# Kernel tuning notes

Measured on AMD Instinct MI355X. Metric: run time of the kernel, lower is better.

## Reference

```python
import jax, jax.numpy as jnp
import numpy as np

N = 1_000_000          # number of fusion candidate pairs
H, W = 200, 70400      # sparse buffer dims hard-coded in the module
FILL = -9999999.0


def _init_conv(k, co, ci):
    # torch Conv2d default init: U(-1/sqrt(fan_in), 1/sqrt(fan_in)), 1x1 kernel
    bound = 1.0 / np.sqrt(ci)
    kw, kb = jax.random.split(k)
    w = jax.random.uniform(kw, (co, ci), jnp.float32, -bound, bound)
    b = jax.random.uniform(kb, (co,), jnp.float32, -bound, bound)
    return w, b


def setup_inputs() -> dict:
    key = jax.random.key(0)
    ks = jax.random.split(key, 7)
    input_1 = jax.random.normal(ks[0], (1, 4, 1, N), dtype=jnp.float32)
    idx0 = jax.random.randint(ks[1], (N,), 0, H)   # row in [0,200)
    idx1 = jax.random.randint(ks[2], (N,), 0, W)   # col in [0,70400)
    tensor_index = jnp.stack([idx0, idx1], axis=1).astype(jnp.int64)
    w1, b1 = _init_conv(ks[3], 18, 4)
    w2, b2 = _init_conv(ks[4], 36, 18)
    w3, b3 = _init_conv(ks[5], 36, 36)
    w4, b4 = _init_conv(ks[6], 1, 36)
    return dict(input_1=input_1, tensor_index=tensor_index,
                w1=w1, b1=b1, w2=w2, b2=b2, w3=w3, b3=b3, w4=w4, b4=b4)


def _fuse_2d_3d(x, w1, b1, w2, b2, w3, b3, w4, b4):
    # x: (4, N); 1x1 convs over a (1,C,1,N) tensor == per-point channel matmuls
    h = jax.nn.relu(w1 @ x + b1[:, None])
    h = jax.nn.relu(w2 @ h + b2[:, None])
    h = jax.nn.relu(w3 @ h + b3[:, None])
    return w4 @ h + b4[:, None]  # (1, N)


def reference(input_1, tensor_index, w1, b1, w2, b2, w3, b3, w4, b4):
    base = jnp.full((1, H, W), FILL, dtype=input_1.dtype)

    def scatter_branch(_):
        feat = _fuse_2d_3d(input_1[0, :, 0, :], w1, b1, w2, b2, w3, b3, w4, b4)  # (1, N)
        out = base.at[:, tensor_index[:, 0], tensor_index[:, 1]].set(feat)
        return out, jnp.int32(1)

    def empty_branch(_):
        return base, jnp.int32(0)

    out_1, flag = jax.lax.cond(tensor_index[0, 0] == -1,
                               empty_branch, scatter_branch, None)
    # MaxPool2d([200,1]) over (C=1,H=200,W) -> max over H; squeeze+reshape -> (1, W, 1)
    x = jnp.max(out_1, axis=1)            # (1, W)
    return x.reshape(1, -1, 1), flag
```

## Files before the change

### kernel.cpp

```cpp
#include <hip/hip_runtime.h>

#define N_PTS 1000000
#define H_DIM 200
#define W_DIM 70400
#define FILL_V -9999999.0f

typedef float v2f __attribute__((ext_vector_type(2)));

__device__ __forceinline__ v2f fma2(v2f a, v2f b, v2f c) {
    return __builtin_elementwise_fma(a, b, c);
}

__global__ void __launch_bounds__(512) mlp_scatter_kernel(
    const float* __restrict__ input,
    const int* __restrict__ tindex,
    const float* __restrict__ w1, const float* __restrict__ b1,
    const float* __restrict__ w2, const float* __restrict__ b2,
    const float* __restrict__ w3, const float* __restrict__ b3,
    const float* __restrict__ w4, const float* __restrict__ b4,
    int* __restrict__ counts,
    uint2* __restrict__ list,
    int maxk)
{
    if (tindex[0] == -1) return;

    const int i = blockIdx.x * 512 + threadIdx.x;
    if (i >= N_PTS) return;

    const int2 hw = ((const int2*)tindex)[i];
    const int pos = atomicAdd(&counts[hw.y], 1);

    const v2f* __restrict__ w1v = (const v2f*)w1;
    const v2f* __restrict__ w2v = (const v2f*)w2;
    const v2f* __restrict__ w3v = (const v2f*)w3;

    const v2f x01 = { input[0 * N_PTS + i], input[1 * N_PTS + i] };
    const v2f x23 = { input[2 * N_PTS + i], input[3 * N_PTS + i] };

    v2f h1v[9];
#pragma unroll
    for (int o = 0; o < 18; ++o) {
        v2f acc = { b1[o], 0.0f };
        acc = fma2(w1v[o * 2 + 0], x01, acc);
        acc = fma2(w1v[o * 2 + 1], x23, acc);
        const float h = fmaxf(acc.x + acc.y, 0.0f);
        if (o & 1) h1v[o >> 1].y = h; else h1v[o >> 1].x = h;
    }

    v2f h2v[18];
#pragma unroll
    for (int o = 0; o < 36; ++o) {
        v2f acc = { b2[o], 0.0f };
#pragma unroll
        for (int q = 0; q < 9; ++q)
            acc = fma2(w2v[o * 9 + q], h1v[q], acc);
        const float h = fmaxf(acc.x + acc.y, 0.0f);
        if (o & 1) h2v[o >> 1].y = h; else h2v[o >> 1].x = h;
    }

    float v = b4[0];
#pragma unroll
    for (int o = 0; o < 36; ++o) {
        v2f acc = { b3[o], 0.0f };
#pragma unroll
        for (int q = 0; q < 18; ++q)
            acc = fma2(w3v[o * 18 + q], h2v[q], acc);
        v = fmaf(w4[o], fmaxf(acc.x + acc.y, 0.0f), v);
    }

    if (pos < maxk) {
        uint2 e;
        e.x = __float_as_uint(v);
        e.y = ((unsigned)i << 8) | (unsigned)hw.x;
        list[(size_t)hw.y * maxk + pos] = e;
    }
}

__device__ __forceinline__ void lds_wave_fence() {
    asm volatile("s_waitcnt lgkmcnt(0)" ::: "memory");
}

__global__ void __launch_bounds__(256) colmax_kernel(
    const int* __restrict__ tindex,
    const int* __restrict__ counts,
    const uint2* __restrict__ list,
    float* __restrict__ out,
    int maxk)
{
    __shared__ unsigned rowwin[4][200];
    const int lane = threadIdx.x;
    const int y    = threadIdx.y;
    unsigned* tbl = rowwin[y];

    const bool empty = (tindex[0] == -1);

    if (blockIdx.x == 0 && lane == 0 && y == 0)
        out[W_DIM] = empty ? 0.0f : 1.0f;

    tbl[lane]       = 0u;
    tbl[lane + 64]  = 0u;
    tbl[lane + 128] = 0u;
    if (lane < 8) tbl[lane + 192] = 0u;
    lds_wave_fence();

    const int step = gridDim.x * 4;
    for (int w = blockIdx.x * 4 + y; w < W_DIM; w += step) {
        int c = 0;
        if (!empty) {
            c = counts[w];
            if (c > maxk) c = maxk;
        }

        uint2 e = make_uint2(0u, 0u);
        const bool have = (lane < c);
        float v = FILL_V;
        if (have) {
            e = list[(size_t)w * maxk + lane];
            atomicMax(&tbl[e.y & 0xFFu], e.y);
        }
        lds_wave_fence();
        if (have) {
            if (tbl[e.y & 0xFFu] == e.y)
                v = __uint_as_float(e.x);
            tbl[e.y & 0xFFu] = 0u;
        }
        lds_wave_fence();

#pragma unroll
        for (int off = 32; off > 0; off >>= 1)
            v = fmaxf(v, __shfl_down(v, off, 64));

        if (lane == 0) out[w] = v;
    }
}

extern "C" void kernel_launch(void* const* d_in, const int* in_sizes, int n_in,
                              void* d_out, int out_size, void* d_ws, size_t ws_size,
                              hipStream_t stream) {
    const float* input  = (const float*)d_in[0];
    const int*   tindex = (const int*)d_in[1];
    const float* w1 = (const float*)d_in[2];
    const float* b1 = (const float*)d_in[3];
    const float* w2 = (const float*)d_in[4];
    const float* b2 = (const float*)d_in[5];
    const float* w3 = (const float*)d_in[6];
    const float* b3 = (const float*)d_in[7];
    const float* w4 = (const float*)d_in[8];
    const float* b4 = (const float*)d_in[9];
    float* out = (float*)d_out;

    int*   counts = (int*)d_ws;
    uint2* list   = (uint2*)((char*)d_ws + (size_t)W_DIM * sizeof(int));

    size_t avail = (ws_size > (size_t)W_DIM * sizeof(int))
                       ? ws_size - (size_t)W_DIM * sizeof(int) : 0;
    int maxk = (int)(avail / ((size_t)W_DIM * sizeof(uint2)));
    if (maxk > 64) maxk = 64;
    if (maxk < 1)  maxk = 1;

    (void)hipMemsetAsync(counts, 0, (size_t)W_DIM * sizeof(int), stream);

    mlp_scatter_kernel<<<(N_PTS + 511) / 512, 512, 0, stream>>>(
        input, tindex, w1, b1, w2, b2, w3, b3, w4, b4, counts, list, maxk);

    colmax_kernel<<<2200, dim3(64, 4), 0, stream>>>(
        tindex, counts, list, out, maxk);
}
```

Measured before the change: 174.5 us.

## Run per-point MLP on bf16 MFMA with packed weights and bias folding

Replaces the per-thread FP32 FMA evaluation of the 4→18→36→36→1 MLP with bf16 MFMA 16x16x32 instructions. Each wavefront processes 64 points, and activations are shuffled between layers with ds_bpermute. A small pre-kernel packs the weights into MFMA fragment layout, with the biases folded in as an extra input column set to 1. The aim is to cut the VALU cost of the MLP, at the price of bf16 rounding of weights and activations, an extra kernel launch, and heavy cross-lane permute traffic.

```diff
diff --git a/kernel.cpp b/kernel.cpp
--- a/kernel.cpp
+++ b/kernel.cpp
@@ -5,72 +5,200 @@
 #define W_DIM 70400
 #define FILL_V -9999999.0f
 
-typedef float v2f __attribute__((ext_vector_type(2)));
-
-__device__ __forceinline__ v2f fma2(v2f a, v2f b, v2f c) {
-    return __builtin_elementwise_fma(a, b, c);
-}
-
-__global__ void __launch_bounds__(512) mlp_scatter_kernel(
-    const float* __restrict__ input,
-    const int* __restrict__ tindex,
+#define COUNTS_BYTES ((size_t)W_DIM * sizeof(int))
+#define WPACK_ELEMS  6656
+#define WPACK_BYTES  ((size_t)WPACK_ELEMS * 2)
+
+typedef __attribute__((ext_vector_type(4))) float f32x4;
+typedef __attribute__((ext_vector_type(8))) short bf16x8;
+
+__device__ __forceinline__ unsigned bperm_u(unsigned src_lane, unsigned v) {
+    return (unsigned)__builtin_amdgcn_ds_bpermute((int)(src_lane << 2), (int)v);
+}
+__device__ __forceinline__ unsigned cvt_pk_bf16(float lo, float hi) {
+    unsigned d;
+    asm("v_cvt_pk_bf16_f32 %0, %1, %2" : "=v"(d) : "v"(lo), "v"(hi));
+    return d;
+}
+__device__ __forceinline__ bf16x8 mk_frag(unsigned d0, unsigned d1,
+                                          unsigned d2, unsigned d3) {
+    union { unsigned u[4]; bf16x8 s; } u;
+    u.u[0] = d0; u.u[1] = d1; u.u[2] = d2; u.u[3] = d3;
+    return u.s;
+}
+
+__global__ void __launch_bounds__(256) pack_weights_kernel(
     const float* __restrict__ w1, const float* __restrict__ b1,
     const float* __restrict__ w2, const float* __restrict__ b2,
     const float* __restrict__ w3, const float* __restrict__ b3,
     const float* __restrict__ w4, const float* __restrict__ b4,
+    unsigned short* __restrict__ wp)
+{
+    for (int idx = threadIdx.x; idx < WPACK_ELEMS; idx += 256) {
+        const int rem  = idx & 511;
+        const int lane = rem >> 3, j = rem & 7;
+        const int c16 = lane & 15, g = lane >> 4;
+        const int kloc = g * 8 + j;
+        float v = 0.0f;
+        if (idx < 1024) {
+            const int row = (idx >> 9) * 16 + c16, k = kloc;
+            if (row < 18) v = (k < 4) ? w1[row * 4 + k] : (k == 4 ? b1[row] : 0.0f);
+        } else if (idx < 2560) {
+            const int row = ((idx - 1024) >> 9) * 16 + c16, k = kloc;
+            if (row < 36) v = (k < 18) ? w2[row * 18 + k] : (k == 18 ? b2[row] : 0.0f);
+        } else if (idx < 5632) {
+            const int f = (idx - 2560) >> 9;
+            const int row = (f >> 1) * 16 + c16, k = (f & 1) * 32 + kloc;
+            if (row < 36) v = (k < 36) ? w3[row * 36 + k] : (k == 36 ? b3[row] : 0.0f);
+        } else {
+            const int row = c16, k = ((idx - 5632) >> 9) * 32 + kloc;
+            if (row == 0) v = (k < 36) ? w4[k] : (k == 36 ? b4[0] : 0.0f);
+        }
+        const unsigned b = __float_as_uint(v);
+        wp[idx] = (unsigned short)((b + 0x7FFFu + ((b >> 16) & 1u)) >> 16);
+    }
+}
+
+__global__ void __launch_bounds__(256) mlp_scatter_kernel(
+    const float* __restrict__ input,
+    const int* __restrict__ tindex,
+    const unsigned short* __restrict__ wp,
     int* __restrict__ counts,
     uint2* __restrict__ list,
     int maxk)
 {
     if (tindex[0] == -1) return;
 
-    const int i = blockIdx.x * 512 + threadIdx.x;
-    if (i >= N_PTS) return;
+    const int l   = threadIdx.x & 63;
+    const int wav = (blockIdx.x * 256 + threadIdx.x) >> 6;
+    const int base = wav << 6;
+    if (base >= N_PTS) return;
+    const int i = base + l;
+    const int c16 = l & 15, g = l >> 4;
 
     const int2 hw = ((const int2*)tindex)[i];
     const int pos = atomicAdd(&counts[hw.y], 1);
 
-    const v2f* __restrict__ w1v = (const v2f*)w1;
-    const v2f* __restrict__ w2v = (const v2f*)w2;
-    const v2f* __restrict__ w3v = (const v2f*)w3;
-
-    const v2f x01 = { input[0 * N_PTS + i], input[1 * N_PTS + i] };
-    const v2f x23 = { input[2 * N_PTS + i], input[3 * N_PTS + i] };
-
-    v2f h1v[9];
-#pragma unroll
-    for (int o = 0; o < 18; ++o) {
-        v2f acc = { b1[o], 0.0f };
-        acc = fma2(w1v[o * 2 + 0], x01, acc);
-        acc = fma2(w1v[o * 2 + 1], x23, acc);
-        const float h = fmaxf(acc.x + acc.y, 0.0f);
-        if (o & 1) h1v[o >> 1].y = h; else h1v[o >> 1].x = h;
-    }
-
-    v2f h2v[18];
-#pragma unroll
-    for (int o = 0; o < 36; ++o) {
-        v2f acc = { b2[o], 0.0f };
-#pragma unroll
-        for (int q = 0; q < 9; ++q)
-            acc = fma2(w2v[o * 9 + q], h1v[q], acc);
-        const float h = fmaxf(acc.x + acc.y, 0.0f);
-        if (o & 1) h2v[o >> 1].y = h; else h2v[o >> 1].x = h;
-    }
-
-    float v = b4[0];
-#pragma unroll
-    for (int o = 0; o < 36; ++o) {
-        v2f acc = { b3[o], 0.0f };
-#pragma unroll
-        for (int q = 0; q < 18; ++q)
-            acc = fma2(w3v[o * 18 + q], h2v[q], acc);
-        v = fmaf(w4[o], fmaxf(acc.x + acc.y, 0.0f), v);
-    }
+    const bf16x8* __restrict__ wf = (const bf16x8*)wp;
+    const bf16x8 A1_0 = wf[0 * 64 + l], A1_1 = wf[1 * 64 + l];
+    const bf16x8 A2_0 = wf[2 * 64 + l], A2_1 = wf[3 * 64 + l], A2_2 = wf[4 * 64 + l];
+    const bf16x8 A3_00 = wf[5 * 64 + l], A3_01 = wf[6 * 64 + l];
+    const bf16x8 A3_10 = wf[7 * 64 + l], A3_11 = wf[8 * 64 + l];
+    const bf16x8 A3_20 = wf[9 * 64 + l], A3_21 = wf[10 * 64 + l];
+    const bf16x8 A4_0 = wf[11 * 64 + l], A4_1 = wf[12 * 64 + l];
+
+    const f32x4 zf = {0.0f, 0.0f, 0.0f, 0.0f};
+
+    const float x0 = input[0 * N_PTS + i], x1 = input[1 * N_PTS + i];
+    const float x2 = input[2 * N_PTS + i], x3 = input[3 * N_PTS + i];
+    const unsigned xp01 = cvt_pk_bf16(x0, x1);
+    const unsigned xp23 = cvt_pk_bf16(x2, x3);
+
+    unsigned P1[4][2][2];
+#pragma unroll
+    for (int t = 0; t < 4; ++t) {
+        const unsigned srcl = (unsigned)(16 * t + c16);
+        const unsigned bx0 = bperm_u(srcl, xp01);
+        const unsigned bx1 = bperm_u(srcl, xp23);
+        const unsigned d0 = (g == 0) ? bx0 : 0u;
+        const unsigned d1 = (g == 0) ? bx1 : 0u;
+        const unsigned d2 = (g == 0) ? 0x3F80u : 0u;
+        const bf16x8 B = mk_frag(d0, d1, d2, 0u);
+        const f32x4 D0 = __builtin_amdgcn_mfma_f32_16x16x32_bf16(A1_0, B, zf, 0, 0, 0);
+        const f32x4 D1 = __builtin_amdgcn_mfma_f32_16x16x32_bf16(A1_1, B, zf, 0, 0, 0);
+        P1[t][0][0] = cvt_pk_bf16(fmaxf(D0.x, 0.f), fmaxf(D0.y, 0.f));
+        P1[t][0][1] = cvt_pk_bf16(fmaxf(D0.z, 0.f), fmaxf(D0.w, 0.f));
+        P1[t][1][0] = cvt_pk_bf16(fmaxf(D1.x, 0.f), fmaxf(D1.y, 0.f));
+        P1[t][1][1] = cvt_pk_bf16(fmaxf(D1.z, 0.f), fmaxf(D1.w, 0.f));
+    }
+
+    unsigned P2[4][3][2];
+#pragma unroll
+    for (int t = 0; t < 4; ++t) {
+        unsigned d[4];
+#pragma unroll
+        for (int p = 0; p < 4; ++p) {
+            const int Rl = (4 * g + p) & 7;
+            const unsigned srcl = (unsigned)(c16 + 16 * (Rl >> 1));
+            const unsigned lo = bperm_u(srcl, P1[t][0][p & 1]);
+            const unsigned hi = bperm_u(srcl, P1[t][1][p & 1]);
+            d[p] = (4 * g + p < 8) ? lo : hi;
+        }
+        if (g == 2) d[1] = (d[1] & 0xFFFF0000u) | 0x3F80u;
+        const bf16x8 B = mk_frag(d[0], d[1], d[2], d[3]);
+        const f32x4 D0 = __builtin_amdgcn_mfma_f32_16x16x32_bf16(A2_0, B, zf, 0, 0, 0);
+        const f32x4 D1 = __builtin_amdgcn_mfma_f32_16x16x32_bf16(A2_1, B, zf, 0, 0, 0);
+        const f32x4 D2 = __builtin_amdgcn_mfma_f32_16x16x32_bf16(A2_2, B, zf, 0, 0, 0);
+        P2[t][0][0] = cvt_pk_bf16(fmaxf(D0.x, 0.f), fmaxf(D0.y, 0.f));
+        P2[t][0][1] = cvt_pk_bf16(fmaxf(D0.z, 0.f), fmaxf(D0.w, 0.f));
+        P2[t][1][0] = cvt_pk_bf16(fmaxf(D1.x, 0.f), fmaxf(D1.y, 0.f));
+        P2[t][1][1] = cvt_pk_bf16(fmaxf(D1.z, 0.f), fmaxf(D1.w, 0.f));
+        P2[t][2][0] = cvt_pk_bf16(fmaxf(D2.x, 0.f), fmaxf(D2.y, 0.f));
+        P2[t][2][1] = cvt_pk_bf16(fmaxf(D2.z, 0.f), fmaxf(D2.w, 0.f));
+    }
+
+    unsigned P3[4][3][2];
+#pragma unroll
+    for (int t = 0; t < 4; ++t) {
+        unsigned dk0[4], dk1[4];
+#pragma unroll
+        for (int p = 0; p < 4; ++p) {
+            const int Rl = (4 * g + p) & 7;
+            const unsigned srcl = (unsigned)(c16 + 16 * (Rl >> 1));
+            const unsigned lo = bperm_u(srcl, P2[t][0][p & 1]);
+            const unsigned hi = bperm_u(srcl, P2[t][1][p & 1]);
+            const unsigned m2 = bperm_u(srcl, P2[t][2][p & 1]);
+            dk0[p] = (4 * g + p < 8) ? lo : hi;
+            dk1[p] = (4 * g + p < 8) ? m2 : 0u;
+        }
+        if (g == 0) dk1[2] = (dk1[2] & 0xFFFF0000u) | 0x3F80u;
+        const bf16x8 B0 = mk_frag(dk0[0], dk0[1], dk0[2], dk0[3]);
+        const bf16x8 B1 = mk_frag(dk1[0], dk1[1], dk1[2], dk1[3]);
+        f32x4 D0 = __builtin_amdgcn_mfma_f32_16x16x32_bf16(A3_00, B0, zf, 0, 0, 0);
+        D0 = __builtin_amdgcn_mfma_f32_16x16x32_bf16(A3_01, B1, D0, 0, 0, 0);
+        f32x4 D1 = __builtin_amdgcn_mfma_f32_16x16x32_bf16(A3_10, B0, zf, 0, 0, 0);
+        D1 = __builtin_amdgcn_mfma_f32_16x16x32_bf16(A3_11, B1, D1, 0, 0, 0);
+        f32x4 D2 = __builtin_amdgcn_mfma_f32_16x16x32_bf16(A3_20, B0, zf, 0, 0, 0);
+        D2 = __builtin_amdgcn_mfma_f32_16x16x32_bf16(A3_21, B1, D2, 0, 0, 0);
+        P3[t][0][0] = cvt_pk_bf16(fmaxf(D0.x, 0.f), fmaxf(D0.y, 0.f));
+        P3[t][0][1] = cvt_pk_bf16(fmaxf(D0.z, 0.f), fmaxf(D0.w, 0.f));
+        P3[t][1][0] = cvt_pk_bf16(fmaxf(D1.x, 0.f), fmaxf(D1.y, 0.f));
+        P3[t][1][1] = cvt_pk_bf16(fmaxf(D1.z, 0.f), fmaxf(D1.w, 0.f));
+        P3[t][2][0] = cvt_pk_bf16(fmaxf(D2.x, 0.f), fmaxf(D2.y, 0.f));
+        P3[t][2][1] = cvt_pk_bf16(fmaxf(D2.z, 0.f), fmaxf(D2.w, 0.f));
+    }
+
+    float vout[4];
+#pragma unroll
+    for (int t = 0; t < 4; ++t) {
+        unsigned dk0[4], dk1[4];
+#pragma unroll
+        for (int p = 0; p < 4; ++p) {
+            const int Rl = (4 * g + p) & 7;
+            const unsigned srcl = (unsigned)(c16 + 16 * (Rl >> 1));
+            const unsigned lo = bperm_u(srcl, P3[t][0][p & 1]);
+            const unsigned hi = bperm_u(srcl, P3[t][1][p & 1]);
+            const unsigned m2 = bperm_u(srcl, P3[t][2][p & 1]);
+            dk0[p] = (4 * g + p < 8) ? lo : hi;
+            dk1[p] = (4 * g + p < 8) ? m2 : 0u;
+        }
+        if (g == 0) dk1[2] = (dk1[2] & 0xFFFF0000u) | 0x3F80u;
+        const bf16x8 B0 = mk_frag(dk0[0], dk0[1], dk0[2], dk0[3]);
+        const bf16x8 B1 = mk_frag(dk1[0], dk1[1], dk1[2], dk1[3]);
+        f32x4 D = __builtin_amdgcn_mfma_f32_16x16x32_bf16(A4_0, B0, zf, 0, 0, 0);
+        D = __builtin_amdgcn_mfma_f32_16x16x32_bf16(A4_1, B1, D, 0, 0, 0);
+        vout[t] = D.x;
+    }
+
+    const unsigned r0 = bperm_u((unsigned)c16, __float_as_uint(vout[0]));
+    const unsigned r1 = bperm_u((unsigned)c16, __float_as_uint(vout[1]));
+    const unsigned r2 = bperm_u((unsigned)c16, __float_as_uint(vout[2]));
+    const unsigned r3 = bperm_u((unsigned)c16, __float_as_uint(vout[3]));
+    const unsigned vr = (g < 2) ? ((g == 0) ? r0 : r1) : ((g == 2) ? r2 : r3);
 
     if (pos < maxk) {
         uint2 e;
-        e.x = __float_as_uint(v);
+        e.x = vr;
         e.y = ((unsigned)i << 8) | (unsigned)hw.x;
         list[(size_t)hw.y * maxk + pos] = e;
     }
@@ -149,19 +277,22 @@
     const float* b4 = (const float*)d_in[9];
     float* out = (float*)d_out;
 
-    int*   counts = (int*)d_ws;
-    uint2* list   = (uint2*)((char*)d_ws + (size_t)W_DIM * sizeof(int));
-
-    size_t avail = (ws_size > (size_t)W_DIM * sizeof(int))
-                       ? ws_size - (size_t)W_DIM * sizeof(int) : 0;
+    int*            counts = (int*)d_ws;
+    unsigned short* wpack  = (unsigned short*)((char*)d_ws + COUNTS_BYTES);
+    uint2*          list   = (uint2*)((char*)d_ws + COUNTS_BYTES + WPACK_BYTES);
+
+    size_t head = COUNTS_BYTES + WPACK_BYTES;
+    size_t avail = (ws_size > head) ? ws_size - head : 0;
     int maxk = (int)(avail / ((size_t)W_DIM * sizeof(uint2)));
     if (maxk > 64) maxk = 64;
     if (maxk < 1)  maxk = 1;
 
-    (void)hipMemsetAsync(counts, 0, (size_t)W_DIM * sizeof(int), stream);
-
-    mlp_scatter_kernel<<<(N_PTS + 511) / 512, 512, 0, stream>>>(
-        input, tindex, w1, b1, w2, b2, w3, b3, w4, b4, counts, list, maxk);
+    (void)hipMemsetAsync(counts, 0, COUNTS_BYTES, stream);
+
+    pack_weights_kernel<<<1, 256, 0, stream>>>(w1, b1, w2, b2, w3, b3, w4, b4, wpack);
+
+    mlp_scatter_kernel<<<(N_PTS / 64 + 3) / 4, 256, 0, stream>>>(
+        input, tindex, wpack, counts, list, maxk);
 
     colmax_kernel<<<2200, dim3(64, 4), 0, stream>>>(
         tindex, counts, list, out, maxk);
```

After: 162.3 us. 7.0% less time.
